# Optimization experiments

Hardware: AMD Instinct MI355X
Metric: run time of the kernel (lower is better)

## Reference

```python
import jax, jax.numpy as jnp
import numpy as np

H = 1024  # hidden_size == embedding_size


def setup_inputs() -> dict:
    key = jax.random.key(0)
    ks = jax.random.split(key, 14)
    B, T, L, V = 2, 1, 8192, 50000
    emb_table = jax.random.normal(ks[0], (V, H), jnp.float32)
    emb_table = emb_table.at[0].set(0.0)  # row 0 zeroed as in the torch module
    return {
        "input_ids": jax.random.randint(ks[1], (B, T), 0, V),
        "last_context": jax.random.normal(ks[2], (B, T, H), jnp.float32),
        "last_hidden": jax.random.normal(ks[3], (1, B, H), jnp.float32),
        "encoder_outputs": jax.random.normal(ks[4], (B, L, H), jnp.float32),
        "emb_table": emb_table,
        "w_ih": jax.random.normal(ks[5], (3 * H, 2 * H), jnp.float32) * 0.02,
        "w_hh": jax.random.normal(ks[6], (3 * H, H), jnp.float32) * 0.02,
        "b_ih": jax.random.normal(ks[7], (3 * H,), jnp.float32) * 0.02,
        "b_hh": jax.random.normal(ks[8], (3 * H,), jnp.float32) * 0.02,
        "attn_w": jax.random.normal(ks[9], (H, 2 * H), jnp.float32) * 0.02,
        "attn_b": jax.random.normal(ks[10], (H,), jnp.float32) * 0.02,
        "v": jax.random.normal(ks[11], (H,), jnp.float32),
        "out_w": jax.random.normal(ks[12], (50000, 2 * H), jnp.float32) * 0.02,
        "out_b": jax.random.normal(ks[13], (50000,), jnp.float32) * 0.02,
    }


def _forward(input_ids, last_context, last_hidden, encoder_outputs, emb_table,
             w_ih, w_hh, b_ih, b_hh, attn_w, attn_b, v, out_w, out_b):
    # Embedding lookup (dropout p=0 -> identity)
    embedded = emb_table[input_ids]                      # [B,1,H]
    rnn_in = jnp.concatenate([embedded, last_context], -1)  # [B,1,2H]

    # Single-step, single-layer GRU (torch gate order: r, z, n)
    x = rnn_in[:, 0]                                     # [B,2H]
    h = last_hidden[0]                                   # [B,H]
    gx = x @ w_ih.T + b_ih                               # [B,3H]
    gh = h @ w_hh.T + b_hh                               # [B,3H]
    r = jax.nn.sigmoid(gx[:, :H] + gh[:, :H])
    z = jax.nn.sigmoid(gx[:, H:2 * H] + gh[:, H:2 * H])
    n = jnp.tanh(gx[:, 2 * H:] + r * gh[:, 2 * H:])
    h_new = (1.0 - z) * n + z * h                        # [B,H]
    rnn_output = h_new[:, None, :]                       # [B,1,H]
    hidden = h_new[None]                                 # [1,B,H]

    # Bahdanau 'concat' attention, vectorized over the seq_len loop:
    # energy[b,i] = v . (attn_w @ concat(h_new[b], enc[b,i]) + attn_b)
    w_h, w_e = attn_w[:, :H], attn_w[:, H:]
    e_h = h_new @ w_h.T + attn_b                         # [B,H]
    e_e = jnp.einsum('blh,kh->blk', encoder_outputs, w_e)  # [B,L,H]
    energies = jnp.einsum('blk,k->bl', e_e + e_h[:, None, :], v)  # [B,L]
    attn_weights = jax.nn.softmax(energies, axis=1)      # [B,L]
    context = jnp.einsum('bl,blh->bh', attn_weights, encoder_outputs)[:, None, :]  # [B,1,H]

    # Output projection over concat(rnn_output, context)
    cat = jnp.concatenate([rnn_output, context], -1)     # [B,1,2H]
    output = cat @ out_w.T + out_b                       # [B,1,V]
    return output, context, hidden, embedded, rnn_output


def reference(input_ids, last_context, last_hidden, encoder_outputs, emb_table,
              w_ih, w_hh, b_ih, b_hh, attn_w, attn_b, v, out_w, out_b):
    return _forward(input_ids, last_context, last_hidden, encoder_outputs, emb_table,
                    w_ih, w_hh, b_ih, b_hh, attn_w, attn_b, v, out_w, out_b)
```

## Files before the change

kernel.cpp:

```cpp
#include <hip/hip_runtime.h>

#define H 1024
#define LEN 8192
#define V 50000
#define NTILE 12500
#define CHUNK 8
#define NCH (LEN / CHUNK)

__device__ __forceinline__ float dot4(float4 a, float4 b) {
    return a.x * b.x + a.y * b.y + a.z * b.z + a.w * b.w;
}

__device__ __forceinline__ void gld_lds16(const float* g, float* l) {
    __builtin_amdgcn_global_load_lds(
        (const __attribute__((address_space(1))) void*)g,
        (__attribute__((address_space(3))) void*)l, 16, 0, 0);
}

__global__ void k_pre(const float* __restrict__ attn_w,
                      const float* __restrict__ v,
                      float* __restrict__ u,
                      const int* __restrict__ ids,
                      const float* __restrict__ emb,
                      float* __restrict__ out_emb,
                      const float* __restrict__ lctx,
                      const float* __restrict__ lhid,
                      const float* __restrict__ w_ih,
                      const float* __restrict__ w_hh,
                      const float* __restrict__ b_ih,
                      const float* __restrict__ b_hh,
                      float* __restrict__ o_hidden,
                      float* __restrict__ o_rnn) {
    __shared__ float red[16][16];
    __shared__ float lds[3][4][4];
    int bid = blockIdx.x;
    int t   = threadIdx.x;

    if (bid < 64) {
        int kg = t >> 4;
        int hi = t & 15;
        int h  = bid * 16 + hi;
        float acc = 0.f;
#pragma unroll 8
        for (int i = 0; i < 64; ++i) {
            int k = kg * 64 + i;
            acc += v[k] * attn_w[(long)k * (2 * H) + H + h];
        }
        red[kg][hi] = acc;
        __syncthreads();
        if (t < 16) {
            float s = 0.f;
#pragma unroll
            for (int g = 0; g < 16; ++g) s += red[g][t];
            u[bid * 16 + t] = s;
        }
        return;
    }
    if (bid < 72) {
        int idx = (bid - 64) * 256 + t;
        int b = idx >> 10, h = idx & 1023;
        out_emb[idx] = emb[(long)ids[b] * H + h];
        return;
    }

    int hh = bid - 72;
    int kb = t * 8;

    float4 x0a, x0b, x1a, x1b;
    if (kb < H) {
        const float* p0 = emb + (long)ids[0] * H + kb;
        const float* p1 = emb + (long)ids[1] * H + kb;
        x0a = *(const float4*)p0;       x0b = *(const float4*)(p0 + 4);
        x1a = *(const float4*)p1;       x1b = *(const float4*)(p1 + 4);
    } else {
        const float* p0 = lctx + (kb - H);
        const float* p1 = lctx + H + (kb - H);
        x0a = *(const float4*)p0;       x0b = *(const float4*)(p0 + 4);
        x1a = *(const float4*)p1;       x1b = *(const float4*)(p1 + 4);
    }
    int kb2 = t * 4;
    float4 h0 = *(const float4*)(lhid + kb2);
    float4 h1 = *(const float4*)(lhid + H + kb2);

    for (int g = 0; g < 3; ++g) {
        const float* wi = w_ih + ((long)g * H + hh) * (2 * H) + kb;
        const float* wh = w_hh + ((long)g * H + hh) * H + kb2;
        float4 wa = *(const float4*)wi;
        float4 wb = *(const float4*)(wi + 4);
        float4 wc = *(const float4*)wh;
        float a0 = dot4(wa, x0a) + dot4(wb, x0b);
        float a1 = dot4(wa, x1a) + dot4(wb, x1b);
        float c0 = dot4(wc, h0);
        float c1 = dot4(wc, h1);
        for (int off = 32; off; off >>= 1) {
            a0 += __shfl_down(a0, off, 64);
            a1 += __shfl_down(a1, off, 64);
            c0 += __shfl_down(c0, off, 64);
            c1 += __shfl_down(c1, off, 64);
        }
        if ((t & 63) == 0) {
            int w = t >> 6;
            lds[g][w][0] = a0; lds[g][w][1] = a1;
            lds[g][w][2] = c0; lds[g][w][3] = c1;
        }
    }
    __syncthreads();
    if (t == 0) {
        float gx[3][2], gh[3][2];
        for (int g = 0; g < 3; ++g) {
            float s0 = 0, s1 = 0, s2 = 0, s3 = 0;
            for (int w = 0; w < 4; ++w) {
                s0 += lds[g][w][0]; s1 += lds[g][w][1];
                s2 += lds[g][w][2]; s3 += lds[g][w][3];
            }
            float bi = b_ih[g * H + hh], bh = b_hh[g * H + hh];
            gx[g][0] = s0 + bi; gx[g][1] = s1 + bi;
            gh[g][0] = s2 + bh; gh[g][1] = s3 + bh;
        }
        for (int b = 0; b < 2; ++b) {
            float r  = 1.f / (1.f + expf(-(gx[0][b] + gh[0][b])));
            float z  = 1.f / (1.f + expf(-(gx[1][b] + gh[1][b])));
            float n  = tanhf(gx[2][b] + r * gh[2][b]);
            float hp = lhid[b * H + hh];
            float hn = (1.f - z) * n + z * hp;
            o_hidden[b * H + hh] = hn;
            o_rnn[b * H + hh]    = hn;
        }
    }
}

__global__ void __launch_bounds__(256)
k_ctx(const float* __restrict__ enc,
      const float* __restrict__ u,
      float* __restrict__ pvec,
      float* __restrict__ marr,
      float* __restrict__ sarr) {
    __shared__ float erow[CHUNK * H];
    __shared__ float elds[CHUNK];
    int t    = threadIdx.x;
    int lane = t & 63;
    int wv   = t >> 6;
    int b    = blockIdx.x >> 10;
    int ch   = blockIdx.x & 1023;

    const float* src = enc + ((long)b * LEN + (long)ch * CHUNK) * H;
#pragma unroll
    for (int i = 0; i < CHUNK; ++i)
        gld_lds16(src + i * H + t * 4, erow + i * H + t * 4);

    float4 uf[4];
#pragma unroll
    for (int c = 0; c < 4; ++c)
        uf[c] = *(const float4*)(u + c * 256 + lane * 4);

    __syncthreads();

#pragma unroll
    for (int rr = 0; rr < 2; ++rr) {
        int r = wv * 2 + rr;
        float acc = 0.f;
#pragma unroll
        for (int c = 0; c < 4; ++c) {
            float4 ev = *(const float4*)(erow + r * H + c * 256 + lane * 4);
            acc += dot4(ev, uf[c]);
        }
        for (int off = 32; off; off >>= 1) acc += __shfl_down(acc, off, 64);
        if (lane == 0) elds[r] = acc;
    }
    __syncthreads();

    float m = elds[0];
#pragma unroll
    for (int r = 1; r < CHUNK; ++r) m = fmaxf(m, elds[r]);
    float p[CHUNK];
    float s = 0.f;
#pragma unroll
    for (int r = 0; r < CHUNK; ++r) { p[r] = expf(elds[r] - m); s += p[r]; }

    float4 acc = {0.f, 0.f, 0.f, 0.f};
#pragma unroll
    for (int r = 0; r < CHUNK; ++r) {
        float4 ev = *(const float4*)(erow + r * H + t * 4);
        acc.x += p[r] * ev.x; acc.y += p[r] * ev.y;
        acc.z += p[r] * ev.z; acc.w += p[r] * ev.w;
    }
    *(float4*)(pvec + (long)blockIdx.x * H + t * 4) = acc;
    if (t == 0) { marr[blockIdx.x] = m; sarr[blockIdx.x] = s; }
}

__global__ void __launch_bounds__(256)
k_red(const float* __restrict__ pvec,
      const float* __restrict__ marr,
      const float* __restrict__ sarr,
      float* __restrict__ out_ctx) {
    __shared__ float scale[NCH];
    __shared__ float red[8][32];
    int t  = threadIdx.x;
    int b  = blockIdx.x >> 5;
    int h0 = (blockIdx.x & 31) * 32;
    const float* mb = marr + b * NCH;
    const float* sb = sarr + b * NCH;

    float m = -3.4e38f;
    for (int i = t; i < NCH; i += 256) m = fmaxf(m, mb[i]);
    for (int off = 32; off; off >>= 1) m = fmaxf(m, __shfl_xor(m, off, 64));
    if ((t & 63) == 0) red[0][t >> 6] = m;
    __syncthreads();
    m = fmaxf(fmaxf(red[0][0], red[0][1]), fmaxf(red[0][2], red[0][3]));
    __syncthreads();

    float d = 0.f;
    for (int i = t; i < NCH; i += 256) {
        float sc = expf(mb[i] - m);
        scale[i] = sc;
        d += sc * sb[i];
    }
    for (int off = 32; off; off >>= 1) d += __shfl_xor(d, off, 64);
    if ((t & 63) == 0) red[0][t >> 6] = d;
    __syncthreads();
    float inv = 1.f / (red[0][0] + red[0][1] + red[0][2] + red[0][3]);
    __syncthreads();

    int grp = t >> 5, il = t & 31;
    const float* pv = pvec + (long)b * NCH * H + (h0 + il);
    float acc = 0.f;
#pragma unroll 4
    for (int c = grp * 128; c < grp * 128 + 128; ++c)
        acc += scale[c] * pv[(long)c * H];
    red[grp][il] = acc;
    __syncthreads();
    if (t < 32) {
        float ssum = 0.f;
#pragma unroll
        for (int g = 0; g < 8; ++g) ssum += red[g][t];
        out_ctx[b * H + h0 + t] = ssum * inv;
    }
}

__global__ void __launch_bounds__(256)
k_out(const float* __restrict__ ow,
      const float* __restrict__ ob,
      const float* __restrict__ hnew,
      const float* __restrict__ ctx,
      float* __restrict__ out) {
    __shared__ float cat[2][2 * H];
    __shared__ float wt[2][4 * 2 * H];
    int t    = threadIdx.x;
    int lane = t & 63;
    int wv   = t >> 6;

    {
        float4* c0 = (float4*)cat[0];
        float4* c1 = (float4*)cat[1];
#pragma unroll
        for (int r = 0; r < 2; ++r) {
            int idx = t + r * 256;
            int k   = idx * 4;
            if (k < H) {
                c0[idx] = *(const float4*)(hnew + k);
                c1[idx] = *(const float4*)(hnew + H + k);
            } else {
                c0[idx] = *(const float4*)(ctx + (k - H));
                c1[idx] = *(const float4*)(ctx + H + (k - H));
            }
        }
    }
    {
        const float* src = ow + (long)blockIdx.x * (4 * 2 * H);
#pragma unroll
        for (int i = 0; i < 8; ++i)
            gld_lds16(src + i * 1024 + t * 4, wt[0] + i * 1024 + t * 4);
    }
    __syncthreads();

    const float4* c0 = (const float4*)cat[0];
    const float4* c1 = (const float4*)cat[1];
    int buf = 0;
    for (int T = blockIdx.x; T < NTILE; T += 512) {
        int Tn = T + 512;
        if (Tn < NTILE) {
            const float* src = ow + (long)Tn * (4 * 2 * H);
            float* dst = wt[buf ^ 1];
#pragma unroll
            for (int i = 0; i < 8; ++i)
                gld_lds16(src + i * 1024 + t * 4, dst + i * 1024 + t * 4);
        }
        const float4* wr = (const float4*)(wt[buf] + wv * (2 * H));
        float a0 = 0.f, a1 = 0.f;
#pragma unroll
        for (int j = 0; j < 8; ++j) {
            float4 w = wr[lane + 64 * j];
            a0 += dot4(w, c0[lane + 64 * j]);
            a1 += dot4(w, c1[lane + 64 * j]);
        }
        for (int off = 32; off; off >>= 1) {
            a0 += __shfl_down(a0, off, 64);
            a1 += __shfl_down(a1, off, 64);
        }
        if (lane == 0) {
            long row = (long)T * 4 + wv;
            float bb = ob[row];
            out[row]     = a0 + bb;
            out[V + row] = a1 + bb;
        }
        __syncthreads();
        buf ^= 1;
    }
}

extern "C" void kernel_launch(void* const* d_in, const int* in_sizes, int n_in,
                              void* d_out, int out_size, void* d_ws, size_t ws_size,
                              hipStream_t stream) {
    const int*   ids    = (const int*)  d_in[0];
    const float* lctx   = (const float*)d_in[1];
    const float* lhid   = (const float*)d_in[2];
    const float* enc    = (const float*)d_in[3];
    const float* emb    = (const float*)d_in[4];
    const float* w_ih   = (const float*)d_in[5];
    const float* w_hh   = (const float*)d_in[6];
    const float* b_ih   = (const float*)d_in[7];
    const float* b_hh   = (const float*)d_in[8];
    const float* attn_w = (const float*)d_in[9];
    const float* v      = (const float*)d_in[11];
    const float* out_w  = (const float*)d_in[12];
    const float* out_b  = (const float*)d_in[13];

    float* out_f       = (float*)d_out;
    float* o_output    = out_f;
    float* o_context   = out_f + 100000;
    float* o_hidden    = out_f + 102048;
    float* o_embedded  = out_f + 104096;
    float* o_rnn       = out_f + 106144;

    float* ws   = (float*)d_ws;
    float* U    = ws;
    float* MARR = ws + 1024;
    float* SARR = ws + 3072;
    float* PVEC = ws + 5120;

    k_pre<<<1096, 256, 0, stream>>>(attn_w, v, U, ids, emb, o_embedded,
                                    lctx, lhid, w_ih, w_hh, b_ih, b_hh,
                                    o_hidden, o_rnn);
    k_ctx<<<2048, 256, 0, stream>>>(enc, U, PVEC, MARR, SARR);
    k_red<<<64,   256, 0, stream>>>(PVEC, MARR, SARR, o_context);
    k_out<<<512,  256, 0, stream>>>(out_w, out_b, o_hidden, o_context,
                                    o_output);
}
```

Before: 115.7 us.

## Split output projection and overlap hidden-half GEMV with attention context kernel

The output projection is split into two halves. The half that multiplies rnn_output by the first H columns of out_w runs inside the attention-context kernel, on every fifth block, and writes partial sums to workspace. A later kernel adds the context half, the bias and the partial. This overlaps streaming half of out_w with streaming encoder_outputs and makes the final kernel read only half the weight. In exchange it writes and reads a partial buffer, mixes two workloads in one grid, and uses larger shared memory in the context blocks, which may lower occupancy.

```diff
diff --git a/kernel.cpp b/kernel.cpp
--- a/kernel.cpp
+++ b/kernel.cpp
@@ -3,9 +3,10 @@
 #define H 1024
 #define LEN 8192
 #define V 50000
-#define NTILE 12500
 #define CHUNK 8
 #define NCH (LEN / CHUNK)
+#define NBH 512
+#define NTH 6250
 
 __device__ __forceinline__ float dot4(float4 a, float4 b) {
     return a.x * b.x + a.y * b.y + a.z * b.z + a.w * b.w;
@@ -130,18 +131,79 @@
 }
 
 __global__ void __launch_bounds__(256)
-k_ctx(const float* __restrict__ enc,
+k_mid(const float* __restrict__ enc,
       const float* __restrict__ u,
       float* __restrict__ pvec,
       float* __restrict__ marr,
-      float* __restrict__ sarr) {
-    __shared__ float erow[CHUNK * H];
-    __shared__ float elds[CHUNK];
+      float* __restrict__ sarr,
+      const float* __restrict__ ow,
+      const float* __restrict__ hnew,
+      float* __restrict__ part) {
+    __shared__ float smem[18432];
     int t    = threadIdx.x;
     int lane = t & 63;
     int wv   = t >> 6;
-    int b    = blockIdx.x >> 10;
-    int ch   = blockIdx.x & 1023;
+    int bid  = blockIdx.x;
+    int r5   = bid % 5;
+    int q5   = bid / 5;
+
+    if (r5 == 0) {
+        float* cat0 = smem;
+        float* cat1 = smem + H;
+        float* wtA  = smem + 2 * H;
+        float* wtB  = smem + 10 * H;
+        ((float4*)cat0)[t] = ((const float4*)hnew)[t];
+        ((float4*)cat1)[t] = ((const float4*)(hnew + H))[t];
+        {
+            const float* srcb = ow + (long)q5 * 8 * (2 * H);
+#pragma unroll
+            for (int i = 0; i < 8; ++i)
+                gld_lds16(srcb + (long)i * (2 * H) + t * 4, wtA + i * H + t * 4);
+        }
+        __syncthreads();
+        int buf = 0;
+        for (int T = q5; T < NTH; T += NBH) {
+            int Tn = T + NBH;
+            if (Tn < NTH) {
+                const float* srcb = ow + (long)Tn * 8 * (2 * H);
+                float* dst = buf ? wtA : wtB;
+#pragma unroll
+                for (int i = 0; i < 8; ++i)
+                    gld_lds16(srcb + (long)i * (2 * H) + t * 4, dst + i * H + t * 4);
+            }
+            const float* w = buf ? wtB : wtA;
+#pragma unroll
+            for (int rr = 0; rr < 2; ++rr) {
+                int r = wv * 2 + rr;
+                const float4* wr = (const float4*)(w + r * H);
+                float a0 = 0.f, a1 = 0.f;
+#pragma unroll
+                for (int j = 0; j < 4; ++j) {
+                    float4 ww = wr[lane + 64 * j];
+                    a0 += dot4(ww, ((const float4*)cat0)[lane + 64 * j]);
+                    a1 += dot4(ww, ((const float4*)cat1)[lane + 64 * j]);
+                }
+                for (int off = 32; off; off >>= 1) {
+                    a0 += __shfl_down(a0, off, 64);
+                    a1 += __shfl_down(a1, off, 64);
+                }
+                if (lane == 0) {
+                    long row = (long)T * 8 + r;
+                    part[row]     = a0;
+                    part[V + row] = a1;
+                }
+            }
+            __syncthreads();
+            buf ^= 1;
+        }
+        return;
+    }
+
+    int cidx = q5 * 4 + (r5 - 1);
+    int b  = cidx >> 10;
+    int ch = cidx & 1023;
+    float* erow = smem;
+    float* elds = smem + CHUNK * H;
 
     const float* src = enc + ((long)b * LEN + (long)ch * CHUNK) * H;
 #pragma unroll
@@ -184,8 +246,8 @@
         acc.x += p[r] * ev.x; acc.y += p[r] * ev.y;
         acc.z += p[r] * ev.z; acc.w += p[r] * ev.w;
     }
-    *(float4*)(pvec + (long)blockIdx.x * H + t * 4) = acc;
-    if (t == 0) { marr[blockIdx.x] = m; sarr[blockIdx.x] = s; }
+    *(float4*)(pvec + (long)cidx * H + t * 4) = acc;
+    if (t == 0) { marr[cidx] = m; sarr[cidx] = s; }
 }
 
 __global__ void __launch_bounds__(256)
@@ -238,70 +300,62 @@
 }
 
 __global__ void __launch_bounds__(256)
-k_out(const float* __restrict__ ow,
-      const float* __restrict__ ob,
-      const float* __restrict__ hnew,
-      const float* __restrict__ ctx,
-      float* __restrict__ out) {
-    __shared__ float cat[2][2 * H];
-    __shared__ float wt[2][4 * 2 * H];
+k_outc(const float* __restrict__ ow,
+       const float* __restrict__ ob,
+       const float* __restrict__ ctx,
+       const float* __restrict__ part,
+       float* __restrict__ out) {
+    __shared__ float smem[18432];
     int t    = threadIdx.x;
     int lane = t & 63;
     int wv   = t >> 6;
-
+    int q    = blockIdx.x;
+
+    float* cat0 = smem;
+    float* cat1 = smem + H;
+    float* wtA  = smem + 2 * H;
+    float* wtB  = smem + 10 * H;
+    ((float4*)cat0)[t] = ((const float4*)ctx)[t];
+    ((float4*)cat1)[t] = ((const float4*)(ctx + H))[t];
     {
-        float4* c0 = (float4*)cat[0];
-        float4* c1 = (float4*)cat[1];
-#pragma unroll
-        for (int r = 0; r < 2; ++r) {
-            int idx = t + r * 256;
-            int k   = idx * 4;
-            if (k < H) {
-                c0[idx] = *(const float4*)(hnew + k);
-                c1[idx] = *(const float4*)(hnew + H + k);
-            } else {
-                c0[idx] = *(const float4*)(ctx + (k - H));
-                c1[idx] = *(const float4*)(ctx + H + (k - H));
-            }
-        }
-    }
-    {
-        const float* src = ow + (long)blockIdx.x * (4 * 2 * H);
+        const float* srcb = ow + (long)q * 8 * (2 * H) + H;
 #pragma unroll
         for (int i = 0; i < 8; ++i)
-            gld_lds16(src + i * 1024 + t * 4, wt[0] + i * 1024 + t * 4);
-    }
-    __syncthreads();
-
-    const float4* c0 = (const float4*)cat[0];
-    const float4* c1 = (const float4*)cat[1];
+            gld_lds16(srcb + (long)i * (2 * H) + t * 4, wtA + i * H + t * 4);
+    }
+    __syncthreads();
     int buf = 0;
-    for (int T = blockIdx.x; T < NTILE; T += 512) {
-        int Tn = T + 512;
-        if (Tn < NTILE) {
-            const float* src = ow + (long)Tn * (4 * 2 * H);
-            float* dst = wt[buf ^ 1];
+    for (int T = q; T < NTH; T += NBH) {
+        int Tn = T + NBH;
+        if (Tn < NTH) {
+            const float* srcb = ow + (long)Tn * 8 * (2 * H) + H;
+            float* dst = buf ? wtA : wtB;
 #pragma unroll
             for (int i = 0; i < 8; ++i)
-                gld_lds16(src + i * 1024 + t * 4, dst + i * 1024 + t * 4);
-        }
-        const float4* wr = (const float4*)(wt[buf] + wv * (2 * H));
-        float a0 = 0.f, a1 = 0.f;
-#pragma unroll
-        for (int j = 0; j < 8; ++j) {
-            float4 w = wr[lane + 64 * j];
-            a0 += dot4(w, c0[lane + 64 * j]);
-            a1 += dot4(w, c1[lane + 64 * j]);
-        }
-        for (int off = 32; off; off >>= 1) {
-            a0 += __shfl_down(a0, off, 64);
-            a1 += __shfl_down(a1, off, 64);
-        }
-        if (lane == 0) {
-            long row = (long)T * 4 + wv;
-            float bb = ob[row];
-            out[row]     = a0 + bb;
-            out[V + row] = a1 + bb;
+                gld_lds16(srcb + (long)i * (2 * H) + t * 4, dst + i * H + t * 4);
+        }
+        const float* w = buf ? wtB : wtA;
+#pragma unroll
+        for (int rr = 0; rr < 2; ++rr) {
+            int r = wv * 2 + rr;
+            const float4* wr = (const float4*)(w + r * H);
+            float a0 = 0.f, a1 = 0.f;
+#pragma unroll
+            for (int j = 0; j < 4; ++j) {
+                float4 ww = wr[lane + 64 * j];
+                a0 += dot4(ww, ((const float4*)cat0)[lane + 64 * j]);
+                a1 += dot4(ww, ((const float4*)cat1)[lane + 64 * j]);
+            }
+            for (int off = 32; off; off >>= 1) {
+                a0 += __shfl_down(a0, off, 64);
+                a1 += __shfl_down(a1, off, 64);
+            }
+            if (lane == 0) {
+                long row = (long)T * 8 + r;
+                float bb = ob[row];
+                out[row]     = part[row]     + a0 + bb;
+                out[V + row] = part[V + row] + a1 + bb;
+            }
         }
         __syncthreads();
         buf ^= 1;
@@ -337,12 +391,13 @@
     float* MARR = ws + 1024;
     float* SARR = ws + 3072;
     float* PVEC = ws + 5120;
-
-    k_pre<<<1096, 256, 0, stream>>>(attn_w, v, U, ids, emb, o_embedded,
-                                    lctx, lhid, w_ih, w_hh, b_ih, b_hh,
-                                    o_hidden, o_rnn);
-    k_ctx<<<2048, 256, 0, stream>>>(enc, U, PVEC, MARR, SARR);
-    k_red<<<64,   256, 0, stream>>>(PVEC, MARR, SARR, o_context);
-    k_out<<<512,  256, 0, stream>>>(out_w, out_b, o_hidden, o_context,
-                                    o_output);
-}
+    float* PART = ws + 5120 + 2048 * 1024;
+
+    k_pre <<<1096, 256, 0, stream>>>(attn_w, v, U, ids, emb, o_embedded,
+                                     lctx, lhid, w_ih, w_hh, b_ih, b_hh,
+                                     o_hidden, o_rnn);
+    k_mid <<<2560, 256, 0, stream>>>(enc, U, PVEC, MARR, SARR,
+                                     out_w, o_hidden, PART);
+    k_red <<<64,   256, 0, stream>>>(PVEC, MARR, SARR, o_context);
+    k_outc<<<512,  256, 0, stream>>>(out_w, out_b, o_context, PART, o_output);
+}
```

Measured after the change: 141.4 us. 22.2% more time.

## Fuse four kernels into one persistent kernel with grid-wide atomic barriers

Applied to the files above, without the earlier changes.

Replaces the four separate launches (GRU/prep, attention chunks, context reduction, output projection) with one persistent kernel of 512 blocks. The stages are separated by software grid barriers built on atomic counters, and a memset resets those counters first. The encoder stage now loops over chunks with LDS double-buffering, and the context reduction is respread so each of the 512 blocks handles 4 output columns. This removes launch gaps and tail effects between stages, at the cost of barrier spin overhead. It relies on all 512 blocks being co-resident, and a guard loop breaks out of the wait if they are not.

```diff
diff --git a/kernel.cpp b/kernel.cpp
--- a/kernel.cpp
+++ b/kernel.cpp
@@ -3,9 +3,10 @@
 #define H 1024
 #define LEN 8192
 #define V 50000
+#define CHUNK 8
+#define NCH 1024
+#define NBLK 512
 #define NTILE 12500
-#define CHUNK 8
-#define NCH (LEN / CHUNK)
 
 __device__ __forceinline__ float dot4(float4 a, float4 b) {
     return a.x * b.x + a.y * b.y + a.z * b.z + a.w * b.w;
@@ -17,294 +18,310 @@
         (__attribute__((address_space(3))) void*)l, 16, 0, 0);
 }
 
-__global__ void k_pre(const float* __restrict__ attn_w,
-                      const float* __restrict__ v,
-                      float* __restrict__ u,
-                      const int* __restrict__ ids,
-                      const float* __restrict__ emb,
-                      float* __restrict__ out_emb,
-                      const float* __restrict__ lctx,
-                      const float* __restrict__ lhid,
-                      const float* __restrict__ w_ih,
-                      const float* __restrict__ w_hh,
-                      const float* __restrict__ b_ih,
-                      const float* __restrict__ b_hh,
-                      float* __restrict__ o_hidden,
-                      float* __restrict__ o_rnn) {
-    __shared__ float red[16][16];
-    __shared__ float lds[3][4][4];
-    int bid = blockIdx.x;
-    int t   = threadIdx.x;
-
-    if (bid < 64) {
-        int kg = t >> 4;
-        int hi = t & 15;
-        int h  = bid * 16 + hi;
-        float acc = 0.f;
-#pragma unroll 8
-        for (int i = 0; i < 64; ++i) {
-            int k = kg * 64 + i;
-            acc += v[k] * attn_w[(long)k * (2 * H) + H + h];
-        }
-        red[kg][hi] = acc;
-        __syncthreads();
-        if (t < 16) {
-            float s = 0.f;
-#pragma unroll
-            for (int g = 0; g < 16; ++g) s += red[g][t];
-            u[bid * 16 + t] = s;
-        }
-        return;
-    }
-    if (bid < 72) {
-        int idx = (bid - 64) * 256 + t;
-        int b = idx >> 10, h = idx & 1023;
-        out_emb[idx] = emb[(long)ids[b] * H + h];
-        return;
-    }
-
-    int hh = bid - 72;
-    int kb = t * 8;
-
-    float4 x0a, x0b, x1a, x1b;
-    if (kb < H) {
-        const float* p0 = emb + (long)ids[0] * H + kb;
-        const float* p1 = emb + (long)ids[1] * H + kb;
-        x0a = *(const float4*)p0;       x0b = *(const float4*)(p0 + 4);
-        x1a = *(const float4*)p1;       x1b = *(const float4*)(p1 + 4);
-    } else {
-        const float* p0 = lctx + (kb - H);
-        const float* p1 = lctx + H + (kb - H);
-        x0a = *(const float4*)p0;       x0b = *(const float4*)(p0 + 4);
-        x1a = *(const float4*)p1;       x1b = *(const float4*)(p1 + 4);
-    }
-    int kb2 = t * 4;
-    float4 h0 = *(const float4*)(lhid + kb2);
-    float4 h1 = *(const float4*)(lhid + H + kb2);
-
-    for (int g = 0; g < 3; ++g) {
-        const float* wi = w_ih + ((long)g * H + hh) * (2 * H) + kb;
-        const float* wh = w_hh + ((long)g * H + hh) * H + kb2;
-        float4 wa = *(const float4*)wi;
-        float4 wb = *(const float4*)(wi + 4);
-        float4 wc = *(const float4*)wh;
-        float a0 = dot4(wa, x0a) + dot4(wb, x0b);
-        float a1 = dot4(wa, x1a) + dot4(wb, x1b);
-        float c0 = dot4(wc, h0);
-        float c1 = dot4(wc, h1);
-        for (int off = 32; off; off >>= 1) {
-            a0 += __shfl_down(a0, off, 64);
-            a1 += __shfl_down(a1, off, 64);
-            c0 += __shfl_down(c0, off, 64);
-            c1 += __shfl_down(c1, off, 64);
-        }
-        if ((t & 63) == 0) {
-            int w = t >> 6;
-            lds[g][w][0] = a0; lds[g][w][1] = a1;
-            lds[g][w][2] = c0; lds[g][w][3] = c1;
-        }
-    }
+__device__ __forceinline__ void stage8k(const float* src, float* dst, int t) {
+#pragma unroll
+    for (int i = 0; i < 8; ++i)
+        gld_lds16(src + i * 1024 + t * 4, dst + i * 1024 + t * 4);
+}
+
+__device__ __forceinline__ void gbar(unsigned* ctr) {
     __syncthreads();
-    if (t == 0) {
-        float gx[3][2], gh[3][2];
-        for (int g = 0; g < 3; ++g) {
-            float s0 = 0, s1 = 0, s2 = 0, s3 = 0;
-            for (int w = 0; w < 4; ++w) {
-                s0 += lds[g][w][0]; s1 += lds[g][w][1];
-                s2 += lds[g][w][2]; s3 += lds[g][w][3];
-            }
-            float bi = b_ih[g * H + hh], bh = b_hh[g * H + hh];
-            gx[g][0] = s0 + bi; gx[g][1] = s1 + bi;
-            gh[g][0] = s2 + bh; gh[g][1] = s3 + bh;
-        }
-        for (int b = 0; b < 2; ++b) {
-            float r  = 1.f / (1.f + expf(-(gx[0][b] + gh[0][b])));
-            float z  = 1.f / (1.f + expf(-(gx[1][b] + gh[1][b])));
-            float n  = tanhf(gx[2][b] + r * gh[2][b]);
-            float hp = lhid[b * H + hh];
-            float hn = (1.f - z) * n + z * hp;
-            o_hidden[b * H + hh] = hn;
-            o_rnn[b * H + hh]    = hn;
-        }
-    }
-}
-
-__global__ void __launch_bounds__(256)
-k_ctx(const float* __restrict__ enc,
-      const float* __restrict__ u,
+    if (threadIdx.x == 0) {
+        __threadfence();
+        __hip_atomic_fetch_add(ctr, 1u, __ATOMIC_ACQ_REL, __HIP_MEMORY_SCOPE_AGENT);
+        long guard = 0;
+        while (__hip_atomic_load(ctr, __ATOMIC_ACQUIRE, __HIP_MEMORY_SCOPE_AGENT)
+               < (unsigned)NBLK) {
+            __builtin_amdgcn_s_sleep(2);
+            if (++guard > (1L << 22)) break;
+        }
+    }
+    __syncthreads();
+}
+
+__global__ void __launch_bounds__(256, 2)
+k_all(const int* __restrict__ ids,
+      const float* __restrict__ emb,
+      const float* __restrict__ lctx,
+      const float* __restrict__ lhid,
+      const float* __restrict__ w_ih,
+      const float* __restrict__ w_hh,
+      const float* __restrict__ b_ih,
+      const float* __restrict__ b_hh,
+      const float* __restrict__ attn_w,
+      const float* __restrict__ v,
+      const float* __restrict__ enc,
+      const float* __restrict__ ow,
+      const float* __restrict__ ob,
+      float* __restrict__ U,
+      float* __restrict__ marr,
+      float* __restrict__ sarr,
       float* __restrict__ pvec,
-      float* __restrict__ marr,
-      float* __restrict__ sarr) {
-    __shared__ float erow[CHUNK * H];
-    __shared__ float elds[CHUNK];
+      unsigned* __restrict__ bar,
+      float* __restrict__ o_output,
+      float* __restrict__ o_context,
+      float* __restrict__ o_hidden,
+      float* __restrict__ o_embedded,
+      float* __restrict__ o_rnn) {
+    __shared__ float smem[16448];
+    float* bufA = smem;
+    float* bufB = smem + 8192;
     int t    = threadIdx.x;
     int lane = t & 63;
     int wv   = t >> 6;
-    int b    = blockIdx.x >> 10;
-    int ch   = blockIdx.x & 1023;
-
-    const float* src = enc + ((long)b * LEN + (long)ch * CHUNK) * H;
-#pragma unroll
-    for (int i = 0; i < CHUNK; ++i)
-        gld_lds16(src + i * H + t * 4, erow + i * H + t * 4);
-
-    float4 uf[4];
-#pragma unroll
-    for (int c = 0; c < 4; ++c)
-        uf[c] = *(const float4*)(u + c * 256 + lane * 4);
-
-    __syncthreads();
-
-#pragma unroll
-    for (int rr = 0; rr < 2; ++rr) {
-        int r = wv * 2 + rr;
-        float acc = 0.f;
-#pragma unroll
-        for (int c = 0; c < 4; ++c) {
-            float4 ev = *(const float4*)(erow + r * H + c * 256 + lane * 4);
-            acc += dot4(ev, uf[c]);
-        }
-        for (int off = 32; off; off >>= 1) acc += __shfl_down(acc, off, 64);
-        if (lane == 0) elds[r] = acc;
-    }
-    __syncthreads();
-
-    float m = elds[0];
-#pragma unroll
-    for (int r = 1; r < CHUNK; ++r) m = fmaxf(m, elds[r]);
-    float p[CHUNK];
-    float s = 0.f;
-#pragma unroll
-    for (int r = 0; r < CHUNK; ++r) { p[r] = expf(elds[r] - m); s += p[r]; }
-
-    float4 acc = {0.f, 0.f, 0.f, 0.f};
-#pragma unroll
-    for (int r = 0; r < CHUNK; ++r) {
-        float4 ev = *(const float4*)(erow + r * H + t * 4);
-        acc.x += p[r] * ev.x; acc.y += p[r] * ev.y;
-        acc.z += p[r] * ev.z; acc.w += p[r] * ev.w;
-    }
-    *(float4*)(pvec + (long)blockIdx.x * H + t * 4) = acc;
-    if (t == 0) { marr[blockIdx.x] = m; sarr[blockIdx.x] = s; }
-}
-
-__global__ void __launch_bounds__(256)
-k_red(const float* __restrict__ pvec,
-      const float* __restrict__ marr,
-      const float* __restrict__ sarr,
-      float* __restrict__ out_ctx) {
-    __shared__ float scale[NCH];
-    __shared__ float red[8][32];
-    int t  = threadIdx.x;
-    int b  = blockIdx.x >> 5;
-    int h0 = (blockIdx.x & 31) * 32;
-    const float* mb = marr + b * NCH;
-    const float* sb = sarr + b * NCH;
-
-    float m = -3.4e38f;
-    for (int i = t; i < NCH; i += 256) m = fmaxf(m, mb[i]);
-    for (int off = 32; off; off >>= 1) m = fmaxf(m, __shfl_xor(m, off, 64));
-    if ((t & 63) == 0) red[0][t >> 6] = m;
-    __syncthreads();
-    m = fmaxf(fmaxf(red[0][0], red[0][1]), fmaxf(red[0][2], red[0][3]));
-    __syncthreads();
-
-    float d = 0.f;
-    for (int i = t; i < NCH; i += 256) {
-        float sc = expf(mb[i] - m);
-        scale[i] = sc;
-        d += sc * sb[i];
-    }
-    for (int off = 32; off; off >>= 1) d += __shfl_xor(d, off, 64);
-    if ((t & 63) == 0) red[0][t >> 6] = d;
-    __syncthreads();
-    float inv = 1.f / (red[0][0] + red[0][1] + red[0][2] + red[0][3]);
-    __syncthreads();
-
-    int grp = t >> 5, il = t & 31;
-    const float* pv = pvec + (long)b * NCH * H + (h0 + il);
-    float acc = 0.f;
-#pragma unroll 4
-    for (int c = grp * 128; c < grp * 128 + 128; ++c)
-        acc += scale[c] * pv[(long)c * H];
-    red[grp][il] = acc;
-    __syncthreads();
-    if (t < 32) {
-        float ssum = 0.f;
-#pragma unroll
-        for (int g = 0; g < 8; ++g) ssum += red[g][t];
-        out_ctx[b * H + h0 + t] = ssum * inv;
-    }
-}
-
-__global__ void __launch_bounds__(256)
-k_out(const float* __restrict__ ow,
-      const float* __restrict__ ob,
-      const float* __restrict__ hnew,
-      const float* __restrict__ ctx,
-      float* __restrict__ out) {
-    __shared__ float cat[2][2 * H];
-    __shared__ float wt[2][4 * 2 * H];
-    int t    = threadIdx.x;
-    int lane = t & 63;
-    int wv   = t >> 6;
+    int bid  = blockIdx.x;
+
+    for (int unit = bid; unit < 1096; unit += NBLK) {
+        if (unit < 1024) {
+            int hh = unit;
+            float* glds = smem;
+            int kb = t * 8;
+            float4 x0a, x0b, x1a, x1b;
+            if (kb < H) {
+                const float* p0 = emb + (long)ids[0] * H + kb;
+                const float* p1 = emb + (long)ids[1] * H + kb;
+                x0a = *(const float4*)p0;  x0b = *(const float4*)(p0 + 4);
+                x1a = *(const float4*)p1;  x1b = *(const float4*)(p1 + 4);
+            } else {
+                const float* p0 = lctx + (kb - H);
+                const float* p1 = lctx + H + (kb - H);
+                x0a = *(const float4*)p0;  x0b = *(const float4*)(p0 + 4);
+                x1a = *(const float4*)p1;  x1b = *(const float4*)(p1 + 4);
+            }
+            int kb2 = t * 4;
+            float4 h0 = *(const float4*)(lhid + kb2);
+            float4 h1 = *(const float4*)(lhid + H + kb2);
+
+            for (int g = 0; g < 3; ++g) {
+                const float* wi = w_ih + ((long)g * H + hh) * (2 * H) + kb;
+                const float* wh = w_hh + ((long)g * H + hh) * H + kb2;
+                float4 wa = *(const float4*)wi;
+                float4 wb = *(const float4*)(wi + 4);
+                float4 wc = *(const float4*)wh;
+                float a0 = dot4(wa, x0a) + dot4(wb, x0b);
+                float a1 = dot4(wa, x1a) + dot4(wb, x1b);
+                float c0 = dot4(wc, h0);
+                float c1 = dot4(wc, h1);
+                for (int off = 32; off; off >>= 1) {
+                    a0 += __shfl_down(a0, off, 64);
+                    a1 += __shfl_down(a1, off, 64);
+                    c0 += __shfl_down(c0, off, 64);
+                    c1 += __shfl_down(c1, off, 64);
+                }
+                if (lane == 0) {
+                    glds[(g * 4 + wv) * 4 + 0] = a0;
+                    glds[(g * 4 + wv) * 4 + 1] = a1;
+                    glds[(g * 4 + wv) * 4 + 2] = c0;
+                    glds[(g * 4 + wv) * 4 + 3] = c1;
+                }
+            }
+            __syncthreads();
+            if (t == 0) {
+                float gx[3][2], gh[3][2];
+                for (int g = 0; g < 3; ++g) {
+                    float s0 = 0, s1 = 0, s2 = 0, s3 = 0;
+                    for (int w = 0; w < 4; ++w) {
+                        s0 += glds[(g * 4 + w) * 4 + 0];
+                        s1 += glds[(g * 4 + w) * 4 + 1];
+                        s2 += glds[(g * 4 + w) * 4 + 2];
+                        s3 += glds[(g * 4 + w) * 4 + 3];
+                    }
+                    float bi = b_ih[g * H + hh], bh = b_hh[g * H + hh];
+                    gx[g][0] = s0 + bi; gx[g][1] = s1 + bi;
+                    gh[g][0] = s2 + bh; gh[g][1] = s3 + bh;
+                }
+                for (int b = 0; b < 2; ++b) {
+                    float r  = 1.f / (1.f + expf(-(gx[0][b] + gh[0][b])));
+                    float z  = 1.f / (1.f + expf(-(gx[1][b] + gh[1][b])));
+                    float n  = tanhf(gx[2][b] + r * gh[2][b]);
+                    float hp = lhid[b * H + hh];
+                    float hn = (1.f - z) * n + z * hp;
+                    o_hidden[b * H + hh] = hn;
+                    o_rnn[b * H + hh]    = hn;
+                }
+            }
+            __syncthreads();
+        } else if (unit < 1088) {
+            int ui = unit - 1024;
+            float* red = smem + 64;
+            int kg = t >> 4, hi = t & 15;
+            int h  = ui * 16 + hi;
+            float acc = 0.f;
+#pragma unroll 8
+            for (int i = 0; i < 64; ++i) {
+                int k = kg * 64 + i;
+                acc += v[k] * attn_w[(long)k * (2 * H) + H + h];
+            }
+            red[kg * 16 + hi] = acc;
+            __syncthreads();
+            if (t < 16) {
+                float s = 0.f;
+#pragma unroll
+                for (int g = 0; g < 16; ++g) s += red[g * 16 + t];
+                U[ui * 16 + t] = s;
+            }
+            __syncthreads();
+        } else {
+            int idx = (unit - 1088) * 256 + t;
+            int b = idx >> 10, h = idx & 1023;
+            o_embedded[idx] = emb[(long)ids[b] * H + h];
+        }
+    }
+    gbar(bar + 0);
 
     {
-        float4* c0 = (float4*)cat[0];
-        float4* c1 = (float4*)cat[1];
-#pragma unroll
-        for (int r = 0; r < 2; ++r) {
-            int idx = t + r * 256;
-            int k   = idx * 4;
-            if (k < H) {
-                c0[idx] = *(const float4*)(hnew + k);
-                c1[idx] = *(const float4*)(hnew + H + k);
+        float4 uf[4];
+#pragma unroll
+        for (int c2 = 0; c2 < 4; ++c2)
+            uf[c2] = *(const float4*)(U + c2 * 256 + lane * 4);
+
+        stage8k(enc + (long)bid * (CHUNK * H), bufA, t);
+        __syncthreads();
+        int buf = 0;
+        for (int c = bid; c < 2 * NCH; c += NBLK) {
+            int cn = c + NBLK;
+            if (cn < 2 * NCH)
+                stage8k(enc + (long)cn * (CHUNK * H), buf ? bufA : bufB, t);
+
+            const float* er = buf ? bufB : bufA;
+            float en8[CHUNK];
+#pragma unroll
+            for (int r = 0; r < CHUNK; ++r) {
+                float acc = 0.f;
+#pragma unroll
+                for (int c2 = 0; c2 < 4; ++c2) {
+                    float4 ev = *(const float4*)(er + r * H + c2 * 256 + lane * 4);
+                    acc += dot4(ev, uf[c2]);
+                }
+#pragma unroll
+                for (int off = 32; off; off >>= 1)
+                    acc += __shfl_xor(acc, off, 64);
+                en8[r] = acc;
+            }
+            float m = en8[0];
+#pragma unroll
+            for (int r = 1; r < CHUNK; ++r) m = fmaxf(m, en8[r]);
+            float p[CHUNK], s = 0.f;
+#pragma unroll
+            for (int r = 0; r < CHUNK; ++r) { p[r] = expf(en8[r] - m); s += p[r]; }
+
+            float4 acc4 = {0.f, 0.f, 0.f, 0.f};
+#pragma unroll
+            for (int r = 0; r < CHUNK; ++r) {
+                float4 ev = *(const float4*)(er + r * H + t * 4);
+                acc4.x += p[r] * ev.x; acc4.y += p[r] * ev.y;
+                acc4.z += p[r] * ev.z; acc4.w += p[r] * ev.w;
+            }
+            *(float4*)(pvec + (long)c * H + t * 4) = acc4;
+            if (t == 0) { marr[c] = m; sarr[c] = s; }
+
+            __syncthreads();
+            buf ^= 1;
+        }
+    }
+    gbar(bar + 1);
+
+    {
+        float* scale = smem;
+        float* rbuf  = smem + 1024;
+        int idx0 = bid * 4;
+        int b  = idx0 >> 10;
+        int hb = idx0 & 1023;
+        const float* mb = marr + b * NCH;
+        const float* sb = sarr + b * NCH;
+
+        float m = -3.4e38f;
+        for (int i = t; i < NCH; i += 256) m = fmaxf(m, mb[i]);
+        for (int off = 32; off; off >>= 1) m = fmaxf(m, __shfl_xor(m, off, 64));
+        if (lane == 0) rbuf[wv] = m;
+        __syncthreads();
+        m = fmaxf(fmaxf(rbuf[0], rbuf[1]), fmaxf(rbuf[2], rbuf[3]));
+        __syncthreads();
+
+        float d = 0.f;
+        for (int i = t; i < NCH; i += 256) {
+            float sc = expf(mb[i] - m);
+            scale[i] = sc;
+            d += sc * sb[i];
+        }
+        for (int off = 32; off; off >>= 1) d += __shfl_xor(d, off, 64);
+        if (lane == 0) rbuf[wv] = d;
+        __syncthreads();
+        float inv = 1.f / (rbuf[0] + rbuf[1] + rbuf[2] + rbuf[3]);
+
+        float4 acc = {0.f, 0.f, 0.f, 0.f};
+        for (int c = t; c < NCH; c += 256) {
+            float sc = scale[c];
+            float4 pv = *(const float4*)(pvec + ((long)b * NCH + c) * H + hb);
+            acc.x += sc * pv.x; acc.y += sc * pv.y;
+            acc.z += sc * pv.z; acc.w += sc * pv.w;
+        }
+        for (int off = 32; off; off >>= 1) {
+            acc.x += __shfl_xor(acc.x, off, 64);
+            acc.y += __shfl_xor(acc.y, off, 64);
+            acc.z += __shfl_xor(acc.z, off, 64);
+            acc.w += __shfl_xor(acc.w, off, 64);
+        }
+        if (lane == 0) *(float4*)(rbuf + 8 + wv * 4) = acc;
+        __syncthreads();
+        if (t == 0) {
+            float4 s0 = *(float4*)(rbuf + 8);
+            float4 s1 = *(float4*)(rbuf + 12);
+            float4 s2 = *(float4*)(rbuf + 16);
+            float4 s3 = *(float4*)(rbuf + 20);
+            float4 r;
+            r.x = (s0.x + s1.x + s2.x + s3.x) * inv;
+            r.y = (s0.y + s1.y + s2.y + s3.y) * inv;
+            r.z = (s0.z + s1.z + s2.z + s3.z) * inv;
+            r.w = (s0.w + s1.w + s2.w + s3.w) * inv;
+            *(float4*)(o_context + idx0) = r;
+        }
+    }
+    gbar(bar + 2);
+
+    {
+        float4 c0[8], c1[8];
+#pragma unroll
+        for (int j = 0; j < 8; ++j) {
+            int k = (lane + 64 * j) * 4;
+            if (j < 4) {
+                c0[j] = *(const float4*)(o_hidden + k);
+                c1[j] = *(const float4*)(o_hidden + H + k);
             } else {
-                c0[idx] = *(const float4*)(ctx + (k - H));
-                c1[idx] = *(const float4*)(ctx + H + (k - H));
-            }
-        }
-    }
-    {
-        const float* src = ow + (long)blockIdx.x * (4 * 2 * H);
-#pragma unroll
-        for (int i = 0; i < 8; ++i)
-            gld_lds16(src + i * 1024 + t * 4, wt[0] + i * 1024 + t * 4);
-    }
-    __syncthreads();
-
-    const float4* c0 = (const float4*)cat[0];
-    const float4* c1 = (const float4*)cat[1];
-    int buf = 0;
-    for (int T = blockIdx.x; T < NTILE; T += 512) {
-        int Tn = T + 512;
-        if (Tn < NTILE) {
-            const float* src = ow + (long)Tn * (4 * 2 * H);
-            float* dst = wt[buf ^ 1];
-#pragma unroll
-            for (int i = 0; i < 8; ++i)
-                gld_lds16(src + i * 1024 + t * 4, dst + i * 1024 + t * 4);
-        }
-        const float4* wr = (const float4*)(wt[buf] + wv * (2 * H));
-        float a0 = 0.f, a1 = 0.f;
-#pragma unroll
-        for (int j = 0; j < 8; ++j) {
-            float4 w = wr[lane + 64 * j];
-            a0 += dot4(w, c0[lane + 64 * j]);
-            a1 += dot4(w, c1[lane + 64 * j]);
-        }
-        for (int off = 32; off; off >>= 1) {
-            a0 += __shfl_down(a0, off, 64);
-            a1 += __shfl_down(a1, off, 64);
-        }
-        if (lane == 0) {
-            long row = (long)T * 4 + wv;
-            float bb = ob[row];
-            out[row]     = a0 + bb;
-            out[V + row] = a1 + bb;
-        }
-        __syncthreads();
-        buf ^= 1;
+                c0[j] = *(const float4*)(o_context + (k - H));
+                c1[j] = *(const float4*)(o_context + H + (k - H));
+            }
+        }
+
+        stage8k(ow + (long)bid * 8192, bufA, t);
+        __syncthreads();
+        int buf = 0;
+        for (int T = bid; T < NTILE; T += NBLK) {
+            int Tn = T + NBLK;
+            if (Tn < NTILE)
+                stage8k(ow + (long)Tn * 8192, buf ? bufA : bufB, t);
+
+            const float4* wr = (const float4*)((buf ? bufB : bufA) + wv * (2 * H));
+            float a0 = 0.f, a1 = 0.f;
+#pragma unroll
+            for (int j = 0; j < 8; ++j) {
+                float4 w = wr[lane + 64 * j];
+                a0 += dot4(w, c0[j]);
+                a1 += dot4(w, c1[j]);
+            }
+            for (int off = 32; off; off >>= 1) {
+                a0 += __shfl_down(a0, off, 64);
+                a1 += __shfl_down(a1, off, 64);
+            }
+            if (lane == 0) {
+                long row = (long)T * 4 + wv;
+                float bb = ob[row];
+                o_output[row]     = a0 + bb;
+                o_output[V + row] = a1 + bb;
+            }
+            __syncthreads();
+            buf ^= 1;
+        }
     }
 }
 
@@ -332,17 +349,18 @@
     float* o_embedded  = out_f + 104096;
     float* o_rnn       = out_f + 106144;
 
-    float* ws   = (float*)d_ws;
-    float* U    = ws;
-    float* MARR = ws + 1024;
-    float* SARR = ws + 3072;
-    float* PVEC = ws + 5120;
-
-    k_pre<<<1096, 256, 0, stream>>>(attn_w, v, U, ids, emb, o_embedded,
-                                    lctx, lhid, w_ih, w_hh, b_ih, b_hh,
-                                    o_hidden, o_rnn);
-    k_ctx<<<2048, 256, 0, stream>>>(enc, U, PVEC, MARR, SARR);
-    k_red<<<64,   256, 0, stream>>>(PVEC, MARR, SARR, o_context);
-    k_out<<<512,  256, 0, stream>>>(out_w, out_b, o_hidden, o_context,
-                                    o_output);
-}
+    float* ws       = (float*)d_ws;
+    unsigned* BAR   = (unsigned*)ws;
+    float* U        = ws + 16;
+    float* MARR     = ws + 16 + 1024;
+    float* SARR     = ws + 16 + 3072;
+    float* PVEC     = ws + 16 + 5120;
+
+    (void)hipMemsetAsync(BAR, 0, 64, stream);
+    k_all<<<NBLK, 256, 0, stream>>>(ids, emb, lctx, lhid, w_ih, w_hh,
+                                    b_ih, b_hh, attn_w, v, enc,
+                                    out_w, out_b,
+                                    U, MARR, SARR, PVEC, BAR,
+                                    o_output, o_context, o_hidden,
+                                    o_embedded, o_rnn);
+}
```

After: 297.9 us. +157.5%, slower.

## Make attention kernel persistent with double-buffered LDS staging and explicit vmcnt waits

Applied to the files above, without the earlier changes.

The context kernel changes from 2048 one-shot blocks to 512 persistent blocks that loop over encoder chunks. Each block double-buffers the chunks in LDS through async global-to-LDS loads, so the next chunk streams in while the current one is processed, and the energy reduction now uses xor shuffles instead of an extra LDS pass. Both streaming kernels replace the full __syncthreads drain with s_waitcnt vmcnt(8) plus a raw s_barrier, so only the previous tile's loads must finish. This relies on correct hand-written vmcnt accounting and gives fewer blocks to hide latency.

```diff
diff --git a/kernel.cpp b/kernel.cpp
--- a/kernel.cpp
+++ b/kernel.cpp
@@ -3,9 +3,10 @@
 #define H 1024
 #define LEN 8192
 #define V 50000
+#define CHUNK 8
+#define NCH 1024
+#define NBLK 512
 #define NTILE 12500
-#define CHUNK 8
-#define NCH (LEN / CHUNK)
 
 __device__ __forceinline__ float dot4(float4 a, float4 b) {
     return a.x * b.x + a.y * b.y + a.z * b.z + a.w * b.w;
@@ -15,6 +16,21 @@
     __builtin_amdgcn_global_load_lds(
         (const __attribute__((address_space(1))) void*)g,
         (__attribute__((address_space(3))) void*)l, 16, 0, 0);
+}
+
+__device__ __forceinline__ void stage8k(const float* src, float* dst, int t) {
+#pragma unroll
+    for (int i = 0; i < 8; ++i)
+        gld_lds16(src + i * 1024 + t * 4, dst + i * 1024 + t * 4);
+}
+
+__device__ __forceinline__ void wait_vm8() {
+    asm volatile("s_waitcnt vmcnt(8)" ::: "memory");
+    __builtin_amdgcn_sched_barrier(0);
+}
+__device__ __forceinline__ void wait_vm0() {
+    asm volatile("s_waitcnt vmcnt(0)" ::: "memory");
+    __builtin_amdgcn_sched_barrier(0);
 }
 
 __global__ void k_pre(const float* __restrict__ attn_w,
@@ -70,13 +86,13 @@
     if (kb < H) {
         const float* p0 = emb + (long)ids[0] * H + kb;
         const float* p1 = emb + (long)ids[1] * H + kb;
-        x0a = *(const float4*)p0;       x0b = *(const float4*)(p0 + 4);
-        x1a = *(const float4*)p1;       x1b = *(const float4*)(p1 + 4);
+        x0a = *(const float4*)p0;  x0b = *(const float4*)(p0 + 4);
+        x1a = *(const float4*)p1;  x1b = *(const float4*)(p1 + 4);
     } else {
         const float* p0 = lctx + (kb - H);
         const float* p1 = lctx + H + (kb - H);
-        x0a = *(const float4*)p0;       x0b = *(const float4*)(p0 + 4);
-        x1a = *(const float4*)p1;       x1b = *(const float4*)(p1 + 4);
+        x0a = *(const float4*)p0;  x0b = *(const float4*)(p0 + 4);
+        x1a = *(const float4*)p1;  x1b = *(const float4*)(p1 + 4);
     }
     int kb2 = t * 4;
     float4 h0 = *(const float4*)(lhid + kb2);
@@ -135,57 +151,66 @@
       float* __restrict__ pvec,
       float* __restrict__ marr,
       float* __restrict__ sarr) {
-    __shared__ float erow[CHUNK * H];
-    __shared__ float elds[CHUNK];
+    __shared__ float bufA[CHUNK * H];
+    __shared__ float bufB[CHUNK * H];
     int t    = threadIdx.x;
     int lane = t & 63;
-    int wv   = t >> 6;
-    int b    = blockIdx.x >> 10;
-    int ch   = blockIdx.x & 1023;
-
-    const float* src = enc + ((long)b * LEN + (long)ch * CHUNK) * H;
-#pragma unroll
-    for (int i = 0; i < CHUNK; ++i)
-        gld_lds16(src + i * H + t * 4, erow + i * H + t * 4);
+    int bid  = blockIdx.x;
 
     float4 uf[4];
 #pragma unroll
-    for (int c = 0; c < 4; ++c)
-        uf[c] = *(const float4*)(u + c * 256 + lane * 4);
-
-    __syncthreads();
-
-#pragma unroll
-    for (int rr = 0; rr < 2; ++rr) {
-        int r = wv * 2 + rr;
-        float acc = 0.f;
-#pragma unroll
-        for (int c = 0; c < 4; ++c) {
-            float4 ev = *(const float4*)(erow + r * H + c * 256 + lane * 4);
-            acc += dot4(ev, uf[c]);
-        }
-        for (int off = 32; off; off >>= 1) acc += __shfl_down(acc, off, 64);
-        if (lane == 0) elds[r] = acc;
-    }
-    __syncthreads();
-
-    float m = elds[0];
-#pragma unroll
-    for (int r = 1; r < CHUNK; ++r) m = fmaxf(m, elds[r]);
-    float p[CHUNK];
-    float s = 0.f;
-#pragma unroll
-    for (int r = 0; r < CHUNK; ++r) { p[r] = expf(elds[r] - m); s += p[r]; }
-
-    float4 acc = {0.f, 0.f, 0.f, 0.f};
-#pragma unroll
-    for (int r = 0; r < CHUNK; ++r) {
-        float4 ev = *(const float4*)(erow + r * H + t * 4);
-        acc.x += p[r] * ev.x; acc.y += p[r] * ev.y;
-        acc.z += p[r] * ev.z; acc.w += p[r] * ev.w;
-    }
-    *(float4*)(pvec + (long)blockIdx.x * H + t * 4) = acc;
-    if (t == 0) { marr[blockIdx.x] = m; sarr[blockIdx.x] = s; }
+    for (int c2 = 0; c2 < 4; ++c2)
+        uf[c2] = *(const float4*)(u + c2 * 256 + lane * 4);
+
+    stage8k(enc + (long)bid * (CHUNK * H), bufA, t);
+    __syncthreads();
+
+    int buf = 0;
+    for (int c = bid; c < 2 * NCH; c += NBLK) {
+        int cn = c + NBLK;
+        if (cn < 2 * NCH) {
+            stage8k(enc + (long)cn * (CHUNK * H), buf ? bufA : bufB, t);
+            wait_vm8();
+        } else {
+            wait_vm0();
+        }
+        __builtin_amdgcn_s_barrier();
+
+        const float* er = buf ? bufB : bufA;
+        float en8[CHUNK];
+#pragma unroll
+        for (int r = 0; r < CHUNK; ++r) {
+            float acc = 0.f;
+#pragma unroll
+            for (int c2 = 0; c2 < 4; ++c2) {
+                float4 ev = *(const float4*)(er + r * H + c2 * 256 + lane * 4);
+                acc += dot4(ev, uf[c2]);
+            }
+#pragma unroll
+            for (int off = 32; off; off >>= 1)
+                acc += __shfl_xor(acc, off, 64);
+            en8[r] = acc;
+        }
+        float m = en8[0];
+#pragma unroll
+        for (int r = 1; r < CHUNK; ++r) m = fmaxf(m, en8[r]);
+        float p[CHUNK], s = 0.f;
+#pragma unroll
+        for (int r = 0; r < CHUNK; ++r) { p[r] = expf(en8[r] - m); s += p[r]; }
+
+        float4 acc4 = {0.f, 0.f, 0.f, 0.f};
+#pragma unroll
+        for (int r = 0; r < CHUNK; ++r) {
+            float4 ev = *(const float4*)(er + r * H + t * 4);
+            acc4.x += p[r] * ev.x; acc4.y += p[r] * ev.y;
+            acc4.z += p[r] * ev.z; acc4.w += p[r] * ev.w;
+        }
+        *(float4*)(pvec + (long)c * H + t * 4) = acc4;
+        if (t == 0) { marr[c] = m; sarr[c] = s; }
+
+        __builtin_amdgcn_s_barrier();
+        buf ^= 1;
+    }
 }
 
 __global__ void __launch_bounds__(256)
@@ -243,15 +268,17 @@
       const float* __restrict__ hnew,
       const float* __restrict__ ctx,
       float* __restrict__ out) {
-    __shared__ float cat[2][2 * H];
-    __shared__ float wt[2][4 * 2 * H];
+    __shared__ float cat0[2 * H];
+    __shared__ float cat1[2 * H];
+    __shared__ float wtA[4 * 2 * H];
+    __shared__ float wtB[4 * 2 * H];
     int t    = threadIdx.x;
     int lane = t & 63;
     int wv   = t >> 6;
 
     {
-        float4* c0 = (float4*)cat[0];
-        float4* c1 = (float4*)cat[1];
+        float4* c0 = (float4*)cat0;
+        float4* c1 = (float4*)cat1;
 #pragma unroll
         for (int r = 0; r < 2; ++r) {
             int idx = t + r * 256;
@@ -264,28 +291,24 @@
                 c1[idx] = *(const float4*)(ctx + H + (k - H));
             }
         }
-    }
-    {
-        const float* src = ow + (long)blockIdx.x * (4 * 2 * H);
-#pragma unroll
-        for (int i = 0; i < 8; ++i)
-            gld_lds16(src + i * 1024 + t * 4, wt[0] + i * 1024 + t * 4);
-    }
-    __syncthreads();
-
-    const float4* c0 = (const float4*)cat[0];
-    const float4* c1 = (const float4*)cat[1];
+        stage8k(ow + (long)blockIdx.x * 8192, wtA, t);
+    }
+    __syncthreads();
+
+    const float4* c0 = (const float4*)cat0;
+    const float4* c1 = (const float4*)cat1;
     int buf = 0;
-    for (int T = blockIdx.x; T < NTILE; T += 512) {
-        int Tn = T + 512;
+    for (int T = blockIdx.x; T < NTILE; T += NBLK) {
+        int Tn = T + NBLK;
         if (Tn < NTILE) {
-            const float* src = ow + (long)Tn * (4 * 2 * H);
-            float* dst = wt[buf ^ 1];
-#pragma unroll
-            for (int i = 0; i < 8; ++i)
-                gld_lds16(src + i * 1024 + t * 4, dst + i * 1024 + t * 4);
-        }
-        const float4* wr = (const float4*)(wt[buf] + wv * (2 * H));
+            stage8k(ow + (long)Tn * 8192, buf ? wtA : wtB, t);
+            wait_vm8();
+        } else {
+            wait_vm0();
+        }
+        __builtin_amdgcn_s_barrier();
+
+        const float4* wr = (const float4*)((buf ? wtB : wtA) + wv * (2 * H));
         float a0 = 0.f, a1 = 0.f;
 #pragma unroll
         for (int j = 0; j < 8; ++j) {
@@ -303,7 +326,7 @@
             out[row]     = a0 + bb;
             out[V + row] = a1 + bb;
         }
-        __syncthreads();
+        __builtin_amdgcn_s_barrier();
         buf ^= 1;
     }
 }
@@ -341,8 +364,8 @@
     k_pre<<<1096, 256, 0, stream>>>(attn_w, v, U, ids, emb, o_embedded,
                                     lctx, lhid, w_ih, w_hh, b_ih, b_hh,
                                     o_hidden, o_rnn);
-    k_ctx<<<2048, 256, 0, stream>>>(enc, U, PVEC, MARR, SARR);
+    k_ctx<<<NBLK, 256, 0, stream>>>(enc, U, PVEC, MARR, SARR);
     k_red<<<64,   256, 0, stream>>>(PVEC, MARR, SARR, o_context);
-    k_out<<<512,  256, 0, stream>>>(out_w, out_b, o_hidden, o_context,
+    k_out<<<NBLK, 256, 0, stream>>>(out_w, out_b, o_hidden, o_context,
                                     o_output);
 }
```

Measured after the change: 122.6 us. +6.0%, slower.
